# Kernel optimization log

Measured on AMD Instinct MI355X. Metric: run time of the kernel, lower is better.

## Reference

```python
import jax, jax.numpy as jnp
import numpy as np

T, B, IN, H, L = 512, 128, 1024, 1024, 4
SCALE = 0.02  # scale randn-init weights so tanh/sigmoid stay in a sane range


def setup_inputs() -> dict:
    key = jax.random.key(0)
    ks = jax.random.split(key, 12)
    f32 = jnp.float32
    return {
        "x": jax.random.normal(ks[0], (T, B, IN), f32),
        "hidden": jax.random.normal(ks[1], (2 * L, B, H), f32) * 0.1,
        "Wii": jax.random.normal(ks[2], (L, 3 * H, IN), f32) * SCALE,
        "Wic": jax.random.normal(ks[3], (L, 3 * H, H), f32) * SCALE,
        "Wih": jax.random.normal(ks[4], (L, 3 * H, H), f32) * SCALE,
        "bii": jax.random.normal(ks[5], (L, 3 * H), f32) * SCALE,
        "bic": jax.random.normal(ks[6], (L, 3 * H), f32) * SCALE,
        "bih": jax.random.normal(ks[7], (L, 3 * H), f32) * SCALE,
        "Whh": jax.random.normal(ks[8], (L, H, H), f32) * SCALE,
        "bhh": jax.random.normal(ks[9], (L, H), f32) * SCALE,
        "Wir": jax.random.normal(ks[10], (L, H, IN), f32) * SCALE,
    }


def _res_lstm_scan(x, hidden, Wii, Wic, Wih, bii, bic, bih, Whh, bhh, Wir):
    n_layers = Wii.shape[0]
    h0, c0 = jnp.split(hidden, 2, axis=0)  # each [L, B, H]

    def step(carry, xt):
        h, c = carry
        out = xt
        new_h, new_c = [], []
        for j in range(n_layers):
            hj, cj = h[j], c[j]
            gates = (out @ Wii[j].T + bii[j]
                     + hj @ Wih[j].T + bih[j]
                     + cj @ Wic[j].T + bic[j])  # [B, 3H]
            i_g, f_g, o_g = jnp.split(gates, 3, axis=1)
            cellgate = jnp.tanh(hj @ Whh[j].T + bhh[j])
            cy = jax.nn.sigmoid(f_g) * cj + jax.nn.sigmoid(i_g) * cellgate
            hy = jax.nn.sigmoid(o_g) * (jnp.tanh(cy) + out @ Wir[j].T)
            out = hy
            new_h.append(hy)
            new_c.append(cy)
        return (jnp.stack(new_h), jnp.stack(new_c)), out

    (hF, cF), outputs = jax.lax.scan(step, (h0, c0), x)
    return outputs, hF, cF


def reference(x, hidden, Wii, Wic, Wih, bii, bic, bih, Whh, bhh, Wir):
    return _res_lstm_scan(x, hidden, Wii, Wic, Wih, bii, bic, bih, Whh, bhh, Wir)
```

## Files before the change

### kernel.cpp

```cpp
#include <hip/hip_runtime.h>


#define TT 512
#define BB 128
#define IN_D 1024
#define HH 1024
#define LL 4
#define G3 3072
#define NSUPER (TT + LL - 1)
#define KC 32
#define NCHUNK 96
#define B_AREA 4096
#define A_AREA 8192
#define BUF_SZ (B_AREA + A_AREA)
#define NBUF 4
#define SLOT (BB * HH)
#define SLOT_ALL (LL * SLOT)

typedef __attribute__((ext_vector_type(8))) __bf16 bf16x8;
typedef __attribute__((ext_vector_type(4))) __bf16 bf16x4;
typedef __attribute__((ext_vector_type(4))) float f32x4;

typedef __attribute__((address_space(3))) void lds_void;
typedef const __attribute__((address_space(1))) void gmem_void;

__device__ __forceinline__ void gload_lds16(const void* g, void* l) {
    __builtin_amdgcn_global_load_lds((gmem_void*)g, (lds_void*)l, 16, 0, 0);
}

__device__ __forceinline__ f32x4 mfma16(bf16x8 a, bf16x8 b, f32x4 c) {
    return __builtin_amdgcn_mfma_f32_16x16x32_bf16(a, b, c, 0, 0, 0);
}

__device__ __forceinline__ int srow(int r) { return (r & 3) ^ ((r >> 2) & 3); }

__device__ __forceinline__ bf16x8 cvt8(float4 u, float4 v) {
    bf16x8 r;
    r[0] = (__bf16)u.x; r[1] = (__bf16)u.y; r[2] = (__bf16)u.z; r[3] = (__bf16)u.w;
    r[4] = (__bf16)v.x; r[5] = (__bf16)v.y; r[6] = (__bf16)v.z; r[7] = (__bf16)v.w;
    return r;
}

__device__ __forceinline__ float sigm(float v) { return 1.f / (1.f + __expf(-v)); }
__device__ __forceinline__ float tanh_fast(float v) { return 1.f - 2.f / (1.f + __expf(2.f * v)); }

__global__ void k_conv_gates(const float* __restrict__ Wii,
                             const float* __restrict__ Wic,
                             const float* __restrict__ Wih,
                             __bf16* __restrict__ Wg) {
    const unsigned total = (unsigned)LL * G3 * G3;
    const unsigned stride = gridDim.x * blockDim.x * 4u;
    for (unsigned idx = (blockIdx.x * blockDim.x + threadIdx.x) * 4u; idx < total; idx += stride) {
        unsigned row = idx / G3;
        int k = (int)(idx - row * G3);
        const float* src; int ks;
        if (k < 1024)      { src = Wii; ks = k; }
        else if (k < 2048) { src = Wih; ks = k - 1024; }
        else               { src = Wic; ks = k - 2048; }
        float4 v = *reinterpret_cast<const float4*>(src + (size_t)row * 1024 + ks);
        bf16x4 o;
        o[0] = (__bf16)v.x; o[1] = (__bf16)v.y; o[2] = (__bf16)v.z; o[3] = (__bf16)v.w;
        *reinterpret_cast<bf16x4*>(Wg + idx) = o;
    }
}

__global__ void k_conv_plain(const float* __restrict__ s, __bf16* __restrict__ d, unsigned total) {
    const unsigned stride = gridDim.x * blockDim.x * 4u;
    for (unsigned idx = (blockIdx.x * blockDim.x + threadIdx.x) * 4u; idx < total; idx += stride) {
        float4 v = *reinterpret_cast<const float4*>(s + idx);
        bf16x4 o;
        o[0] = (__bf16)v.x; o[1] = (__bf16)v.y; o[2] = (__bf16)v.z; o[3] = (__bf16)v.w;
        *reinterpret_cast<bf16x4*>(d + idx) = o;
    }
}

__global__ void k_bias(const float* __restrict__ bii, const float* __restrict__ bic,
                       const float* __restrict__ bih, const float* __restrict__ bhh,
                       float* __restrict__ bsum) {
    int i = blockIdx.x * blockDim.x + threadIdx.x;
    int j = i >> 12, n = i & 4095;
    if (j >= LL) return;
    if (n < G3) bsum[j * 4096 + n] = bii[j * G3 + n] + bih[j * G3 + n] + bic[j * G3 + n];
    else        bsum[j * 4096 + n] = bhh[j * HH + (n - G3)];
}

__global__ void k_init(const float* __restrict__ hidden,
                       float* __restrict__ cbufF, __bf16* __restrict__ hb, __bf16* __restrict__ cb) {
    const unsigned stride = gridDim.x * blockDim.x;
    for (unsigned i = blockIdx.x * blockDim.x + threadIdx.x; i < SLOT_ALL; i += stride) {
        float hv = hidden[i];
        float cv = hidden[SLOT_ALL + i];
        hb[SLOT_ALL + i] = (__bf16)hv;
        cb[SLOT_ALL + i] = (__bf16)cv;
        cbufF[SLOT_ALL + i] = cv;
    }
}

__global__ void k_final(const float* __restrict__ hfin, const float* __restrict__ cbufF,
                        float* __restrict__ out_tail) {
    const unsigned stride = gridDim.x * blockDim.x;
    for (unsigned i = blockIdx.x * blockDim.x + threadIdx.x; i < SLOT_ALL; i += stride) {
        out_tail[i] = hfin[i];
        out_tail[SLOT_ALL + i] = cbufF[SLOT_ALL + i];
    }
}

__global__ __launch_bounds__(512) void k_super(
    const float* __restrict__ x,
    const __bf16* __restrict__ Wg,
    const __bf16* __restrict__ Whh,
    const __bf16* __restrict__ Wir,
    const float* __restrict__ bsum,
    float* __restrict__ cbufF,
    __bf16* __restrict__ hb,
    __bf16* __restrict__ cb,
    float* __restrict__ hfin,
    float* __restrict__ dout,
    int s)
{
    const int j = blockIdx.y;
    const int t = s - j;
    if (t < 0 || t >= TT) return;

    __shared__ __align__(16) char smem[NBUF * BUF_SZ];

    const int p = t & 1, pp = p ^ 1;
    const float*  csrcF = cbufF + (size_t)pp * SLOT_ALL + (size_t)j * SLOT;
    float*        cdstF = cbufF + (size_t)p  * SLOT_ALL + (size_t)j * SLOT;
    const __bf16* panH = hb + (size_t)pp * SLOT_ALL + (size_t)j * SLOT;
    const __bf16* panC = cb + (size_t)pp * SLOT_ALL + (size_t)j * SLOT;
    const __bf16* panO = hb + (size_t)p * SLOT_ALL + (size_t)(j - 1) * SLOT;
    __bf16* hdstB = hb + (size_t)p * SLOT_ALL + (size_t)j * SLOT;
    __bf16* cdstB = cb + (size_t)p * SLOT_ALL + (size_t)j * SLOT;

    const int tid  = threadIdx.x;
    const int lane = tid & 63;
    const int wave = tid >> 6;
    const int lrow = lane & 15;
    const int kgrp = lane >> 4;
    const int n0 = blockIdx.x * 16;
    const int m0 = wave * 16;

    const int bs_row = lane >> 2;
    const int bs_phys = lane & 3;
    const int bs_k8 = ((bs_phys ^ srow(bs_row)) << 3);
    const __bf16* Wgj = Wg + (size_t)j * G3 * G3;
    const __bf16* st_g  = Wgj + (size_t)(wave * 1024 + n0 + bs_row) * G3 + bs_k8;
    const __bf16* st_wr = Wir + (size_t)j * HH * IN_D + (size_t)(n0 + bs_row) * IN_D + bs_k8;
    const __bf16* st_wc = Whh + (size_t)j * HH * HH + (size_t)(n0 + bs_row) * HH + bs_k8;
    const int bs_dst = wave * 1024 + lane * 16;

    const int ao = (wave - 4) * 2;
    const int as_rowin = lane >> 2;
    const int as_phys = lane & 3;
    const int as_k8 = ((as_phys ^ srow(as_rowin)) << 3);
    const int as_row0 = ao * 16 + as_rowin;
    const size_t paoff0 = (size_t)as_row0 * HH + as_k8;
    const size_t paoff1 = paoff0 + (size_t)16 * HH;
    const int as_dst0 = B_AREA + ao * 1024 + lane * 16;
    const int as_dst1 = as_dst0 + 1024;

    const int bswz = ((kgrp ^ srow(lrow)) << 4);
    const int boff0 = 0 * 1024 + lrow * 64 + bswz;
    const int boff1 = 1 * 1024 + lrow * 64 + bswz;
    const int boff2 = 2 * 1024 + lrow * 64 + bswz;
    const int boff3 = 3 * 1024 + lrow * 64 + bswz;
    const int aoff = B_AREA + (m0 + lrow) * 64 + bswz;

    const float* aX = x + (size_t)t * SLOT + (size_t)(m0 + lrow) * IN_D + kgrp * 8;

    auto stage = [&](int c) {
        if (c >= NCHUNK) return;
        const int rg = c >> 5;
        const int kk = (c & 31) << 5;
        char* buf = smem + (c & 3) * BUF_SZ;
        if (wave < 3) {
            gload_lds16(st_g + rg * 1024 + kk, buf + bs_dst);
        } else if (wave == 3) {
            if (rg == 0)      gload_lds16(st_wr + kk, buf + bs_dst);
            else              gload_lds16(st_wc + kk, buf + bs_dst);
        } else {
            if (rg == 0) {
                if (j > 0) {
                    gload_lds16(panO + paoff0 + kk, buf + as_dst0);
                    gload_lds16(panO + paoff1 + kk, buf + as_dst1);
                }
            } else if (rg == 1) {
                gload_lds16(panH + paoff0 + kk, buf + as_dst0);
                gload_lds16(panH + paoff1 + kk, buf + as_dst1);
            } else {
                gload_lds16(panC + paoff0 + kk, buf + as_dst0);
                gload_lds16(panC + paoff1 + kk, buf + as_dst1);
            }
        }
    };

    f32x4 vi = {0,0,0,0}, vf = {0,0,0,0}, vo = {0,0,0,0}, vc = {0,0,0,0}, vr = {0,0,0,0};

    float4 x0, x1;
    if (j == 0) { x0 = *(const float4*)(aX); x1 = *(const float4*)(aX + 4); }

    stage(0); stage(1); stage(2);
    if (wave < 4) asm volatile("s_waitcnt vmcnt(2)" ::: "memory");
    else          asm volatile("s_waitcnt vmcnt(4)" ::: "memory");
    __builtin_amdgcn_s_barrier();

    for (int c = 0; c < NCHUNK; ++c) {
        const int rg = c >> 5;
        char* buf = smem + (c & 3) * BUF_SZ;

        bf16x8 a;
        if (j == 0 && rg == 0) {
            a = cvt8(x0, x1);
            if (c + 1 < 32) {
                const float* px = aX + ((c + 1) << 5);
                x0 = *(const float4*)(px); x1 = *(const float4*)(px + 4);
            }
        } else {
            a = *(const bf16x8*)(buf + aoff);
        }

        stage(c + 3);

        bf16x8 b;
        b = *(const bf16x8*)(buf + boff0); vi = mfma16(a, b, vi);
        b = *(const bf16x8*)(buf + boff1); vf = mfma16(a, b, vf);
        b = *(const bf16x8*)(buf + boff2); vo = mfma16(a, b, vo);
        if (rg == 0)      { b = *(const bf16x8*)(buf + boff3); vr = mfma16(a, b, vr); }
        else if (rg == 1) { b = *(const bf16x8*)(buf + boff3); vc = mfma16(a, b, vc); }

        if (wave < 4) asm volatile("s_waitcnt vmcnt(2)" ::: "memory");
        else          asm volatile("s_waitcnt vmcnt(4)" ::: "memory");
        __builtin_amdgcn_s_barrier();
    }

    const int col = n0 + lrow;
    const float b_i = bsum[j * 4096 + col];
    const float b_f = bsum[j * 4096 + HH + col];
    const float b_o = bsum[j * 4096 + 2 * HH + col];
    const float b_c = bsum[j * 4096 + G3 + col];

    #pragma unroll
    for (int r = 0; r < 4; ++r) {
        const int m = m0 + kgrp * 4 + r;
        const size_t o = (size_t)m * HH + col;
        float iv = vi[r] + b_i;
        float fv = vf[r] + b_f;
        float ov = vo[r] + b_o;
        float cg = tanh_fast(vc[r] + b_c);
        float cold = csrcF[o];
        float cy = sigm(fv) * cold + sigm(iv) * cg;
        float hy = sigm(ov) * (tanh_fast(cy) + vr[r]);
        cdstF[o] = cy;
        cdstB[o] = (__bf16)cy;
        hdstB[o] = (__bf16)hy;
        if (t == TT - 1) hfin[(size_t)j * SLOT + o] = hy;
        if (j == LL - 1) dout[(size_t)t * SLOT + o] = hy;
    }
}

extern "C" void kernel_launch(void* const* d_in, const int* in_sizes, int n_in,
                              void* d_out, int out_size, void* d_ws, size_t ws_size,
                              hipStream_t stream) {
    const float* x      = (const float*)d_in[0];
    const float* hidden = (const float*)d_in[1];
    const float* Wii    = (const float*)d_in[2];
    const float* Wic    = (const float*)d_in[3];
    const float* Wih    = (const float*)d_in[4];
    const float* bii    = (const float*)d_in[5];
    const float* bic    = (const float*)d_in[6];
    const float* bih    = (const float*)d_in[7];
    const float* Whh    = (const float*)d_in[8];
    const float* bhh    = (const float*)d_in[9];
    const float* Wir    = (const float*)d_in[10];
    float* out = (float*)d_out;

    char* ws = (char*)d_ws;
    __bf16* Wg    = (__bf16*)(ws);
    __bf16* Whh_b = (__bf16*)(ws + 75497472);
    __bf16* Wir_b = (__bf16*)(ws + 83886080);
    float*  cbufF = (float*)(ws + 92274688);
    float*  bsum  = (float*)(ws + 96468992);
    __bf16* hb    = (__bf16*)(ws + 96534528);
    __bf16* cb    = (__bf16*)(ws + 98631680);
    float*  hfin  = (float*)(ws + 100728832);

    k_conv_gates<<<4096, 256, 0, stream>>>(Wii, Wic, Wih, Wg);
    k_conv_plain<<<2048, 256, 0, stream>>>(Whh, Whh_b, (unsigned)(LL * HH * HH));
    k_conv_plain<<<2048, 256, 0, stream>>>(Wir, Wir_b, (unsigned)(LL * HH * IN_D));
    k_bias<<<64, 256, 0, stream>>>(bii, bic, bih, bhh, bsum);
    k_init<<<1024, 256, 0, stream>>>(hidden, cbufF, hb, cb);

    dim3 grid(64, LL), block(512);
    for (int s = 0; s < NSUPER; ++s)
        k_super<<<grid, block, 0, stream>>>(x, Wg, Whh_b, Wir_b, bsum,
                                            cbufF, hb, cb, hfin, out, s);

    k_final<<<1024, 256, 0, stream>>>(hfin, cbufF, out + (size_t)TT * SLOT);
}
```

Before: 36.18 ms.

## Restructure super-step kernel: 4 waves, larger K granules, A operand from global

Halves the block to 256 threads, and each wave now computes two 16-row M fragments so every B tile read from LDS feeds two MFMAs. Weight tiles are staged in 128-wide K granules (24 instead of 96 chunks), so there are far fewer barriers per step. The A operand (h/c/previous-layer activations or x) is now loaded straight from global into registers instead of through LDS. This trades more register pressure and uncoalesced or latency-exposed A loads from global for less LDS staging and synchronisation overhead.

```diff
diff --git a/kernel.cpp b/kernel.cpp
--- a/kernel.cpp
+++ b/kernel.cpp
@@ -8,11 +8,8 @@
 #define LL 4
 #define G3 3072
 #define NSUPER (TT + LL - 1)
-#define KC 32
-#define NCHUNK 96
-#define B_AREA 4096
-#define A_AREA 8192
-#define BUF_SZ (B_AREA + A_AREA)
+#define NGRAN 24
+#define GBUF 16384
 #define NBUF 4
 #define SLOT (BB * HH)
 #define SLOT_ALL (LL * SLOT)
@@ -31,8 +28,6 @@
 __device__ __forceinline__ f32x4 mfma16(bf16x8 a, bf16x8 b, f32x4 c) {
     return __builtin_amdgcn_mfma_f32_16x16x32_bf16(a, b, c, 0, 0, 0);
 }
-
-__device__ __forceinline__ int srow(int r) { return (r & 3) ^ ((r >> 2) & 3); }
 
 __device__ __forceinline__ bf16x8 cvt8(float4 u, float4 v) {
     bf16x8 r;
@@ -105,7 +100,7 @@
     }
 }
 
-__global__ __launch_bounds__(512) void k_super(
+__global__ __launch_bounds__(256) void k_super(
     const float* __restrict__ x,
     const __bf16* __restrict__ Wg,
     const __bf16* __restrict__ Whh,
@@ -122,116 +117,126 @@
     const int t = s - j;
     if (t < 0 || t >= TT) return;
 
-    __shared__ __align__(16) char smem[NBUF * BUF_SZ];
+    __shared__ __align__(16) char smem[NBUF * GBUF];
 
     const int p = t & 1, pp = p ^ 1;
     const float*  csrcF = cbufF + (size_t)pp * SLOT_ALL + (size_t)j * SLOT;
     float*        cdstF = cbufF + (size_t)p  * SLOT_ALL + (size_t)j * SLOT;
     const __bf16* panH = hb + (size_t)pp * SLOT_ALL + (size_t)j * SLOT;
     const __bf16* panC = cb + (size_t)pp * SLOT_ALL + (size_t)j * SLOT;
-    const __bf16* panO = hb + (size_t)p * SLOT_ALL + (size_t)(j - 1) * SLOT;
+    const __bf16* panO = (j == 0) ? panH
+                                  : hb + (size_t)p * SLOT_ALL + (size_t)(j - 1) * SLOT;
     __bf16* hdstB = hb + (size_t)p * SLOT_ALL + (size_t)j * SLOT;
     __bf16* cdstB = cb + (size_t)p * SLOT_ALL + (size_t)j * SLOT;
 
     const int tid  = threadIdx.x;
     const int lane = tid & 63;
-    const int wave = tid >> 6;
+    const int w    = tid >> 6;
     const int lrow = lane & 15;
     const int kgrp = lane >> 4;
-    const int n0 = blockIdx.x * 16;
-    const int m0 = wave * 16;
-
-    const int bs_row = lane >> 2;
-    const int bs_phys = lane & 3;
-    const int bs_k8 = ((bs_phys ^ srow(bs_row)) << 3);
+    const int row4 = lane >> 4;
+    const int slot = lane & 15;
+    const int n0   = blockIdx.x * 16;
+
     const __bf16* Wgj = Wg + (size_t)j * G3 * G3;
-    const __bf16* st_g  = Wgj + (size_t)(wave * 1024 + n0 + bs_row) * G3 + bs_k8;
-    const __bf16* st_wr = Wir + (size_t)j * HH * IN_D + (size_t)(n0 + bs_row) * IN_D + bs_k8;
-    const __bf16* st_wc = Whh + (size_t)j * HH * HH + (size_t)(n0 + bs_row) * HH + bs_k8;
-    const int bs_dst = wave * 1024 + lane * 16;
-
-    const int ao = (wave - 4) * 2;
-    const int as_rowin = lane >> 2;
-    const int as_phys = lane & 3;
-    const int as_k8 = ((as_phys ^ srow(as_rowin)) << 3);
-    const int as_row0 = ao * 16 + as_rowin;
-    const size_t paoff0 = (size_t)as_row0 * HH + as_k8;
-    const size_t paoff1 = paoff0 + (size_t)16 * HH;
-    const int as_dst0 = B_AREA + ao * 1024 + lane * 16;
-    const int as_dst1 = as_dst0 + 1024;
-
-    const int bswz = ((kgrp ^ srow(lrow)) << 4);
-    const int boff0 = 0 * 1024 + lrow * 64 + bswz;
-    const int boff1 = 1 * 1024 + lrow * 64 + bswz;
-    const int boff2 = 2 * 1024 + lrow * 64 + bswz;
-    const int boff3 = 3 * 1024 + lrow * 64 + bswz;
-    const int aoff = B_AREA + (m0 + lrow) * 64 + bswz;
-
-    const float* aX = x + (size_t)t * SLOT + (size_t)(m0 + lrow) * IN_D + kgrp * 8;
-
-    auto stage = [&](int c) {
-        if (c >= NCHUNK) return;
-        const int rg = c >> 5;
-        const int kk = (c & 31) << 5;
-        char* buf = smem + (c & 3) * BUF_SZ;
-        if (wave < 3) {
-            gload_lds16(st_g + rg * 1024 + kk, buf + bs_dst);
-        } else if (wave == 3) {
-            if (rg == 0)      gload_lds16(st_wr + kk, buf + bs_dst);
-            else              gload_lds16(st_wc + kk, buf + bs_dst);
+    const __bf16* bA[4];
+    const __bf16* bB[4];
+    #pragma unroll
+    for (int o = 0; o < 4; ++o) {
+        const int row = 4 * o + row4;
+        const int kel = (slot ^ (row & 7)) << 3;
+        if (w < 3) {
+            bA[o] = Wgj + (size_t)(w * 1024 + n0 + row) * G3 + kel;
+            bB[o] = bA[o];
         } else {
-            if (rg == 0) {
-                if (j > 0) {
-                    gload_lds16(panO + paoff0 + kk, buf + as_dst0);
-                    gload_lds16(panO + paoff1 + kk, buf + as_dst1);
-                }
-            } else if (rg == 1) {
-                gload_lds16(panH + paoff0 + kk, buf + as_dst0);
-                gload_lds16(panH + paoff1 + kk, buf + as_dst1);
-            } else {
-                gload_lds16(panC + paoff0 + kk, buf + as_dst0);
-                gload_lds16(panC + paoff1 + kk, buf + as_dst1);
+            bA[o] = Wir + (size_t)j * HH * IN_D + (size_t)(n0 + row) * IN_D + kel;
+            bB[o] = Whh + (size_t)j * HH * HH  + (size_t)(n0 + row) * HH  + kel;
+        }
+    }
+    char* st_dst0 = smem + w * 4096 + (lane << 4);
+
+    auto stage = [&](int g) {
+        if (g >= NGRAN) return;
+        const int rg = g >> 3;
+        char* dst = st_dst0 + (g & 3) * GBUF;
+        const long gkw = (w < 3) ? ((long)g << 7) : ((long)(g & 7) << 7);
+        #pragma unroll
+        for (int o = 0; o < 4; ++o)
+            gload_lds16(((rg == 0) ? bA[o] : bB[o]) + gkw, dst + o * 1024);
+    };
+
+    const __bf16* pH0 = panH + (size_t)(32 * w + lrow) * HH;
+    const __bf16* pH1 = pH0 + (size_t)16 * HH;
+    const __bf16* pC0 = panC + (size_t)(32 * w + lrow) * HH;
+    const __bf16* pC1 = pC0 + (size_t)16 * HH;
+    const __bf16* pO0 = panO + (size_t)(32 * w + lrow) * HH;
+    const __bf16* pO1 = pO0 + (size_t)16 * HH;
+    const float*  xr0 = x + (size_t)t * SLOT + (size_t)(32 * w + lrow) * IN_D;
+    const float*  xr1 = xr0 + (size_t)16 * IN_D;
+    const int kg8 = kgrp << 3;
+
+    f32x4 vi[2] = {{0,0,0,0},{0,0,0,0}}, vf_[2] = {{0,0,0,0},{0,0,0,0}},
+          vo[2] = {{0,0,0,0},{0,0,0,0}}, vc[2] = {{0,0,0,0},{0,0,0,0}},
+          vr[2] = {{0,0,0,0},{0,0,0,0}};
+
+    stage(0); stage(1); stage(2);
+    asm volatile("s_waitcnt vmcnt(8)" ::: "memory");
+    __builtin_amdgcn_s_barrier();
+
+    for (int g = 0; g < NGRAN; ++g) {
+        const int rg = g >> 3;
+        const int kw = (g & 7) << 7;
+        const char* buf = smem + (g & 3) * GBUF;
+        const bool xpath = (j == 0) & (rg == 0);
+
+        bf16x8 ab0[4], ab1[4];
+        float4 xq0a[4], xq0b[4], xq1a[4], xq1b[4];
+        if (xpath) {
+            #pragma unroll
+            for (int cc = 0; cc < 4; ++cc) {
+                const int ko = kw + cc * 32 + kg8;
+                xq0a[cc] = *(const float4*)(xr0 + ko);
+                xq0b[cc] = *(const float4*)(xr0 + ko + 4);
+                xq1a[cc] = *(const float4*)(xr1 + ko);
+                xq1b[cc] = *(const float4*)(xr1 + ko + 4);
+            }
+        } else {
+            const __bf16* r0 = (rg == 0) ? pO0 : (rg == 1) ? pH0 : pC0;
+            const __bf16* r1 = (rg == 0) ? pO1 : (rg == 1) ? pH1 : pC1;
+            #pragma unroll
+            for (int cc = 0; cc < 4; ++cc) {
+                const int ko = kw + cc * 32 + kg8;
+                ab0[cc] = *(const bf16x8*)(r0 + ko);
+                ab1[cc] = *(const bf16x8*)(r1 + ko);
             }
         }
-    };
-
-    f32x4 vi = {0,0,0,0}, vf = {0,0,0,0}, vo = {0,0,0,0}, vc = {0,0,0,0}, vr = {0,0,0,0};
-
-    float4 x0, x1;
-    if (j == 0) { x0 = *(const float4*)(aX); x1 = *(const float4*)(aX + 4); }
-
-    stage(0); stage(1); stage(2);
-    if (wave < 4) asm volatile("s_waitcnt vmcnt(2)" ::: "memory");
-    else          asm volatile("s_waitcnt vmcnt(4)" ::: "memory");
-    __builtin_amdgcn_s_barrier();
-
-    for (int c = 0; c < NCHUNK; ++c) {
-        const int rg = c >> 5;
-        char* buf = smem + (c & 3) * BUF_SZ;
-
-        bf16x8 a;
-        if (j == 0 && rg == 0) {
-            a = cvt8(x0, x1);
-            if (c + 1 < 32) {
-                const float* px = aX + ((c + 1) << 5);
-                x0 = *(const float4*)(px); x1 = *(const float4*)(px + 4);
+
+        stage(g + 3);
+
+        #pragma unroll
+        for (int cc = 0; cc < 4; ++cc) {
+            const int sw = ((cc * 4 + kgrp) ^ (lrow & 7)) << 4;
+            const char* bb = buf + (lrow << 8) + sw;
+            bf16x8 a0 = xpath ? cvt8(xq0a[cc], xq0b[cc]) : ab0[cc];
+            bf16x8 a1 = xpath ? cvt8(xq1a[cc], xq1b[cc]) : ab1[cc];
+            bf16x8 b0 = *(const bf16x8*)(bb);
+            bf16x8 b1 = *(const bf16x8*)(bb + 4096);
+            bf16x8 b2 = *(const bf16x8*)(bb + 8192);
+            vi[0] = mfma16(a0, b0, vi[0]);  vi[1] = mfma16(a1, b0, vi[1]);
+            vf_[0] = mfma16(a0, b1, vf_[0]); vf_[1] = mfma16(a1, b1, vf_[1]);
+            vo[0] = mfma16(a0, b2, vo[0]);  vo[1] = mfma16(a1, b2, vo[1]);
+            if (rg == 0) {
+                bf16x8 b3 = *(const bf16x8*)(bb + 12288);
+                vr[0] = mfma16(a0, b3, vr[0]); vr[1] = mfma16(a1, b3, vr[1]);
+            } else if (rg == 1) {
+                bf16x8 b3 = *(const bf16x8*)(bb + 12288);
+                vc[0] = mfma16(a0, b3, vc[0]); vc[1] = mfma16(a1, b3, vc[1]);
             }
-        } else {
-            a = *(const bf16x8*)(buf + aoff);
         }
 
-        stage(c + 3);
-
-        bf16x8 b;
-        b = *(const bf16x8*)(buf + boff0); vi = mfma16(a, b, vi);
-        b = *(const bf16x8*)(buf + boff1); vf = mfma16(a, b, vf);
-        b = *(const bf16x8*)(buf + boff2); vo = mfma16(a, b, vo);
-        if (rg == 0)      { b = *(const bf16x8*)(buf + boff3); vr = mfma16(a, b, vr); }
-        else if (rg == 1) { b = *(const bf16x8*)(buf + boff3); vc = mfma16(a, b, vc); }
-
-        if (wave < 4) asm volatile("s_waitcnt vmcnt(2)" ::: "memory");
-        else          asm volatile("s_waitcnt vmcnt(4)" ::: "memory");
-        __builtin_amdgcn_s_barrier();
+        if (g == NGRAN - 2)     { asm volatile("s_waitcnt vmcnt(0)" ::: "memory"); }
+        else if (g < NGRAN - 2) { asm volatile("s_waitcnt vmcnt(8)" ::: "memory"); }
+        if (g < NGRAN - 1) __builtin_amdgcn_s_barrier();
     }
 
     const int col = n0 + lrow;
@@ -241,21 +246,24 @@
     const float b_c = bsum[j * 4096 + G3 + col];
 
     #pragma unroll
-    for (int r = 0; r < 4; ++r) {
-        const int m = m0 + kgrp * 4 + r;
-        const size_t o = (size_t)m * HH + col;
-        float iv = vi[r] + b_i;
-        float fv = vf[r] + b_f;
-        float ov = vo[r] + b_o;
-        float cg = tanh_fast(vc[r] + b_c);
-        float cold = csrcF[o];
-        float cy = sigm(fv) * cold + sigm(iv) * cg;
-        float hy = sigm(ov) * (tanh_fast(cy) + vr[r]);
-        cdstF[o] = cy;
-        cdstB[o] = (__bf16)cy;
-        hdstB[o] = (__bf16)hy;
-        if (t == TT - 1) hfin[(size_t)j * SLOT + o] = hy;
-        if (j == LL - 1) dout[(size_t)t * SLOT + o] = hy;
+    for (int f = 0; f < 2; ++f) {
+        #pragma unroll
+        for (int r = 0; r < 4; ++r) {
+            const int m = 32 * w + 16 * f + kgrp * 4 + r;
+            const size_t o = (size_t)m * HH + col;
+            float iv = vi[f][r] + b_i;
+            float fv = vf_[f][r] + b_f;
+            float ov = vo[f][r] + b_o;
+            float cg = tanh_fast(vc[f][r] + b_c);
+            float cold = csrcF[o];
+            float cy = sigm(fv) * cold + sigm(iv) * cg;
+            float hy = sigm(ov) * (tanh_fast(cy) + vr[f][r]);
+            cdstF[o] = cy;
+            cdstB[o] = (__bf16)cy;
+            hdstB[o] = (__bf16)hy;
+            if (t == TT - 1) hfin[(size_t)j * SLOT + o] = hy;
+            if (j == LL - 1) dout[(size_t)t * SLOT + o] = hy;
+        }
     }
 }
 
@@ -291,7 +299,7 @@
     k_bias<<<64, 256, 0, stream>>>(bii, bic, bih, bhh, bsum);
     k_init<<<1024, 256, 0, stream>>>(hidden, cbufF, hb, cb);
 
-    dim3 grid(64, LL), block(512);
+    dim3 grid(64, LL), block(256);
     for (int s = 0; s < NSUPER; ++s)
         k_super<<<grid, block, 0, stream>>>(x, Wg, Whh_b, Wir_b, bsum,
                                             cbufF, hb, cb, hfin, out, s);
```

After: 37.17 ms. 2.7% more time.
